# Performance work log

Measured on AMD Instinct MI355X. Metric: run time of the kernel, lower is better.

The kernel has to match this reference:

```python
import jax, jax.numpy as jnp
import numpy as np

# graph structure constants
G = 64            # num graphs
NPG = 1600        # nodes per graph
N = G * NPG       # 102400 total nodes
EPG = 51200       # edges per graph (avg degree 32)
E = G * EPG       # 3276800 total edges
F_IN = 512
H_OUT = 512
RATIO = 0.8
K = int(np.ceil(RATIO * NPG))   # 1280 kept nodes per graph
NK = G * K


def gcn_conv(x, src, dst, W, b, n, ew):
    """PyG GCNConv: D^-1/2 (A+I) D^-1/2 X W + b, with edge weights ew."""
    h = x @ W
    deg = jax.ops.segment_sum(ew, dst, num_segments=n) + 1.0  # +1 for self loop
    dis = jax.lax.rsqrt(deg)
    norm = dis[src] * dis[dst] * ew                 # [E]
    agg = jax.ops.segment_sum(h[src] * norm[:, None], dst, num_segments=n)
    return agg + h * (dis * dis)[:, None] + b       # self-loop norm = dis_i^2


def setup_inputs() -> dict:
    key = jax.random.key(0)
    k_x, k_e, k_w1, k_wr, k_wo, k_w2 = jax.random.split(key, 6)
    x = jax.random.normal(k_x, (N, F_IN), dtype=jnp.float32)
    # within-graph random edges
    local = jax.random.randint(k_e, (2, G, EPG), 0, NPG, dtype=jnp.int32)
    offs = (jnp.arange(G, dtype=jnp.int32) * NPG)[None, :, None]
    edge_index = (local + offs).reshape(2, E)
    batch = jnp.repeat(jnp.arange(G, dtype=jnp.int32), NPG)
    W1 = jax.random.normal(k_w1, (F_IN, 16), dtype=jnp.float32) * (1.0 / np.sqrt(F_IN))
    b1 = jnp.zeros((16,), jnp.float32)
    Wrel = jax.random.normal(k_wr, (16, 1), dtype=jnp.float32) * 0.25
    brel = jnp.zeros((1,), jnp.float32)
    Wroot = jax.random.normal(k_wo, (16, 1), dtype=jnp.float32) * 0.25
    W2 = jax.random.normal(k_w2, (16, H_OUT), dtype=jnp.float32) * 0.25
    b2 = jnp.zeros((H_OUT,), jnp.float32)
    return {"x": x, "edge_index": edge_index, "batch": batch,
            "W1": W1, "b1": b1, "Wrel": Wrel, "brel": brel,
            "Wroot": Wroot, "W2": W2, "b2": b2}


def reference(x, edge_index, batch, W1, b1, Wrel, brel, Wroot, W2, b2):
    src, dst = edge_index[0], edge_index[1]
    ones_e = jnp.ones((E,), x.dtype)
    # conv1 + relu
    h1 = jax.nn.relu(gcn_conv(x, src, dst, W1, b1, N, ones_e))   # [N,16]
    # SAGPooling score: GraphConv(16,1) = lin_rel(sum_j x_j) + lin_root(x), then tanh
    agg = jax.ops.segment_sum(h1[src], dst, num_segments=N)
    score = jnp.tanh((agg @ Wrel + brel + h1 @ Wroot)[:, 0])      # [N]
    # per-graph top-k (graphs are equal-sized, contiguous)
    vals, idx = jax.lax.top_k(score.reshape(G, NPG), K)           # [G,K]
    perm = (idx + (jnp.arange(G, dtype=idx.dtype) * NPG)[:, None]).reshape(-1)  # [NK]
    xk = h1[perm] * vals.reshape(-1)[:, None]                     # x[perm] * score[perm]
    # filter_adj: keep edges with both endpoints kept, remap indices
    kept = jnp.zeros((N,), bool).at[perm].set(True)
    inv = jnp.zeros((N,), jnp.int32).at[perm].set(jnp.arange(NK, dtype=jnp.int32))
    em = (kept[src] & kept[dst]).astype(x.dtype)                  # weight-0 == dropped edge
    # conv2 + relu on pooled graph
    h2 = jax.nn.relu(gcn_conv(xk, inv[src], inv[dst], W2, b2, NK, em))  # [NK,H]
    # global mean pool (each graph keeps exactly K nodes)
    out = jax.ops.segment_sum(h2, batch[perm], num_segments=G) / K
    return out
```

## Files before the change

### kernel.cpp

```cpp
#include <hip/hip_runtime.h>
#include <math.h>

#define G_    64
#define NPG_  1600
#define N_    (G_*NPG_)
#define EPG_  51200
#define E_    (G_*EPG_)
#define FIN_  512
#define HOUT_ 512
#define KEEP_ 1280

__global__ __launch_bounds__(1024) void k_build(const int* __restrict__ esrc,
                                                const int* __restrict__ edst,
                                                int* __restrict__ offs,
                                                int* __restrict__ rend,
                                                float* __restrict__ dis,
                                                unsigned short* __restrict__ csr) {
  __shared__ __align__(16) unsigned short csrs[EPG_];
  __shared__ int hist[NPG_];
  __shared__ int wsum[16];
  const int g = blockIdx.x, t = threadIdx.x;
  const int lane = t & 63, wid = t >> 6;
  const int eb = g * EPG_, nb = g * NPG_;

  for (int i = t; i < NPG_; i += 1024) hist[i] = 0;
  __syncthreads();
  for (int e = t; e < EPG_; e += 1024) atomicAdd(&hist[edst[eb + e] - nb], 1);
  __syncthreads();

  int c0 = 0, c1 = 0;
  if (t < 800) { c0 = hist[2 * t]; c1 = hist[2 * t + 1]; }
  const int val = c0 + c1;
  int incl = val;
#pragma unroll
  for (int m = 1; m < 64; m <<= 1) {
    const int u = __shfl_up(incl, m);
    if (lane >= m) incl += u;
  }
  if (lane == 63) wsum[wid] = incl;
  __syncthreads();
  int woff = 0;
  for (int w2 = 0; w2 < wid; ++w2) woff += wsum[w2];
  incl += woff;
  if (t < 800) {
    const int excl = incl - val;
    const int p0 = excl, p1 = p0 + c0;
    offs[nb + 2 * t] = eb + p0;     rend[nb + 2 * t] = eb + p1;
    offs[nb + 2 * t + 1] = eb + p1; rend[nb + 2 * t + 1] = eb + p1 + c1;
    dis[nb + 2 * t] = rsqrtf((float)c0 + 1.0f);
    dis[nb + 2 * t + 1] = rsqrtf((float)c1 + 1.0f);
    hist[2 * t] = p0;
    hist[2 * t + 1] = p1;
  }
  __syncthreads();
  for (int e = t; e < EPG_; e += 1024) {
    const int s = esrc[eb + e];
    const int d = edst[eb + e] - nb;
    const int p = atomicAdd(&hist[d], 1);
    csrs[p] = (unsigned short)(s - nb);
  }
  __syncthreads();
  const uint4* s4 = reinterpret_cast<const uint4*>(csrs);
  uint4* d4 = reinterpret_cast<uint4*>(csr + eb);
  for (int i = t; i < EPG_ / 8; i += 1024) d4[i] = s4[i];
}

typedef _Float16 f16x8 __attribute__((ext_vector_type(8)));
typedef float f32x4 __attribute__((ext_vector_type(4)));
#define WSTR_ 520

__global__ __launch_bounds__(256, 4) void k_xw1(const float* __restrict__ x,
                                                const float* __restrict__ W1,
                                                const float* __restrict__ dis,
                                                float* __restrict__ hd) {
  __shared__ _Float16 wls[2][16][WSTR_];
  const int t = threadIdx.x;

  for (int i = t; i < FIN_ * 16; i += 256) {
    const int k = i >> 4, n = i & 15;
    const float w = W1[i];
    const _Float16 w1 = (_Float16)w;
    const float r = w - (float)w1;
    wls[0][n][k] = w1;
    wls[1][n][k] = (_Float16)r;
  }
  __syncthreads();

  const int lane = t & 63, wid = t >> 6;
  const int g = lane >> 4, m = lane & 15;
  const int tile = blockIdx.x * 4 + wid;
  const int rb = tile * 16;

  const float* xrow = x + (size_t)(rb + m) * FIN_ + g * 8;
  const _Float16* wb1 = &wls[0][m][g * 8];
  const _Float16* wb2 = &wls[1][m][g * 8];

  f32x4 acc = {0.f, 0.f, 0.f, 0.f};
#pragma unroll
  for (int t4 = 0; t4 < 16; ++t4) {
    const float4 p0 = *reinterpret_cast<const float4*>(xrow + t4 * 32);
    const float4 p1 = *reinterpret_cast<const float4*>(xrow + t4 * 32 + 4);
    const float xv[8] = {p0.x, p0.y, p0.z, p0.w, p1.x, p1.y, p1.z, p1.w};
    f16x8 a1, a2;
#pragma unroll
    for (int j = 0; j < 8; ++j) {
      const _Float16 h = (_Float16)xv[j];
      a1[j] = h;
      a2[j] = (_Float16)(xv[j] - (float)h);
    }
    const f16x8 b1 = *reinterpret_cast<const f16x8*>(wb1 + t4 * 32);
    const f16x8 b2 = *reinterpret_cast<const f16x8*>(wb2 + t4 * 32);
    acc = __builtin_amdgcn_mfma_f32_16x16x32_f16(a1, b1, acc, 0, 0, 0);
    acc = __builtin_amdgcn_mfma_f32_16x16x32_f16(a1, b2, acc, 0, 0, 0);
    acc = __builtin_amdgcn_mfma_f32_16x16x32_f16(a2, b1, acc, 0, 0, 0);
  }

  const float4 d4 = reinterpret_cast<const float4*>(dis)[(rb >> 2) + g];
  const float dd[4] = {d4.x, d4.y, d4.z, d4.w};
#pragma unroll
  for (int rg = 0; rg < 4; ++rg)
    hd[(size_t)(rb + g * 4 + rg) * 16 + m] = acc[rg] * dd[rg];
}

__global__ __launch_bounds__(1024) void k_conv1l(
    const unsigned short* __restrict__ csr, const int* __restrict__ offs,
    const int* __restrict__ rend, const float* __restrict__ hd,
    const float* __restrict__ dis, const float* __restrict__ b1,
    const float* __restrict__ Wrel, const float* __restrict__ Wroot,
    float* __restrict__ h1, float* __restrict__ rarr, float* __restrict__ tarr) {
  __shared__ float hds[NPG_ * 16];
  const int g = blockIdx.x >> 2, q = blockIdx.x & 3;
  const int nb = g * NPG_;
  const int t = threadIdx.x;
  {
    const float4* src = reinterpret_cast<const float4*>(hd + (size_t)nb * 16);
    float4* dst = reinterpret_cast<float4*>(hds);
    for (int i = t; i < NPG_ * 4; i += 1024) dst[i] = src[i];
  }
  __syncthreads();
  const int c = t & 15;
  const float bb = b1[c], wr = Wrel[c], wo = Wroot[c];
  const int vend = q * 400 + 400;
  for (int vl = q * 400 + (t >> 4); vl < vend; vl += 64) {
    const int v = nb + vl;
    const int rs = offs[v], re = rend[v];
    float acc = 0.f;
    int k = rs;
    for (; k + 4 <= re; k += 4) {
      const int s0 = csr[k], s1 = csr[k + 1];
      const int s2 = csr[k + 2], s3 = csr[k + 3];
      acc += hds[s0 * 16 + c] + hds[s1 * 16 + c];
      acc += hds[s2 * 16 + c] + hds[s3 * 16 + c];
    }
    for (; k < re; ++k) acc += hds[csr[k] * 16 + c];
    const float dd = dis[v];
    float val = fmaf(acc + hds[vl * 16 + c], dd, bb);
    val = fmaxf(val, 0.f);
    h1[(size_t)v * 16 + c] = val;
    float r = val * wr;
    float tt = val * wo;
#pragma unroll
    for (int m = 1; m < 16; m <<= 1) {
      r += __shfl_xor(r, m);
      tt += __shfl_xor(tt, m);
    }
    if (c == 0) { rarr[v] = r; tarr[v] = tt; }
  }
}

__global__ __launch_bounds__(320) void k_score(
    const unsigned short* __restrict__ csr, const int* __restrict__ offs,
    const int* __restrict__ rend, const float* __restrict__ rarr,
    const float* __restrict__ tarr, const float* __restrict__ brel,
    float* __restrict__ scoreg, unsigned* __restrict__ uug) {
  __shared__ float rar[NPG_];
  const int g = blockIdx.x / 5, q = blockIdx.x % 5;
  const int nb = g * NPG_;
  const int t = threadIdx.x;
  for (int i = t; i < NPG_; i += 320) rar[i] = rarr[nb + i];
  __syncthreads();
  const int vl = q * 320 + t;
  const int v = nb + vl;
  const int rs = offs[v], re = rend[v];
  float sum = 0.f;
  int k = rs;
  for (; k + 4 <= re; k += 4) {
    sum += rar[csr[k]] + rar[csr[k + 1]];
    sum += rar[csr[k + 2]] + rar[csr[k + 3]];
  }
  for (; k < re; ++k) sum += rar[csr[k]];
  const float s = tanhf(sum + brel[0] + tarr[v]);
  scoreg[v] = s;
  const unsigned ub = __float_as_uint(s);
  uug[v] = (ub & 0x80000000u) ? ~ub : (ub | 0x80000000u);
}

__global__ __launch_bounds__(1024) void k_topk(
    const unsigned* __restrict__ uug, int* __restrict__ kept,
    float* __restrict__ out) {
  __shared__ unsigned uu[NPG_];
  __shared__ int kp[NPG_];
  __shared__ int hist[256];
  __shared__ int part[16];
  __shared__ int scal[2];
  const int g = blockIdx.x, t = threadIdx.x;
  const int lane = t & 63, wid = t >> 6;
  const int nb = g * NPG_;

  for (int i = t; i < NPG_; i += 1024) uu[i] = uug[nb + i];
  if (t == 0) { scal[0] = 0; scal[1] = KEEP_; }
  __syncthreads();

  const unsigned maskTab[4] = {0u, 0xFF000000u, 0xFFFF0000u, 0xFFFFFF00u};
  const int shTab[4] = {24, 16, 8, 0};
  for (int pass = 0; pass < 4; ++pass) {
    const unsigned lo = (unsigned)scal[0];
    const int remc = scal[1];
    const unsigned msk = maskTab[pass];
    const int sh = shTab[pass];
    if (t < 256) hist[t] = 0;
    __syncthreads();
    for (int v = t; v < NPG_; v += 1024) {
      const unsigned u = uu[v];
      if (((u ^ lo) & msk) == 0) atomicAdd(&hist[(u >> sh) & 255], 1);
    }
    __syncthreads();
    int hv = 0;
    if (t < 256) hv = hist[t];
    int incl = hv;
#pragma unroll
    for (int m = 1; m < 64; m <<= 1) {
      const int u2 = __shfl_up(incl, m);
      if (lane >= m) incl += u2;
    }
    if (t < 256 && lane == 63) part[wid] = incl;
    __syncthreads();
    if (t < 256) {
      int woff = 0;
      for (int w2 = 0; w2 < wid; ++w2) woff += part[w2];
      const int tot = part[0] + part[1] + part[2] + part[3];
      const int sb = tot - (incl + woff) + hv;
      const int sb1 = sb - hv;
      if (sb >= remc && sb1 < remc) {
        scal[0] = (int)(lo | ((unsigned)t << sh));
        scal[1] = remc - sb1;
      }
    }
    __syncthreads();
  }
  const unsigned T = (unsigned)scal[0];
  const int remT = scal[1];

  const int i0 = 2 * t, i1 = 2 * t + 1;
  int f0 = 0, f1 = 0;
  if (i0 < NPG_) f0 = (uu[i0] == T);
  if (i1 < NPG_) f1 = (uu[i1] == T);
  int incl2 = f0 + f1;
#pragma unroll
  for (int m = 1; m < 64; m <<= 1) {
    const int u2 = __shfl_up(incl2, m);
    if (lane >= m) incl2 += u2;
  }
  if (lane == 63) part[wid] = incl2;
  __syncthreads();
  int woff2 = 0;
  for (int w2 = 0; w2 < wid; ++w2) woff2 += part[w2];
  const int excl = incl2 + woff2 - (f0 + f1);
  if (i0 < NPG_) kp[i0] = (uu[i0] > T) || (f0 && excl < remT);
  if (i1 < NPG_) kp[i1] = (uu[i1] > T) || (f1 && (excl + f0) < remT);
  __syncthreads();
  for (int v = t; v < NPG_; v += 1024) kept[nb + v] = kp[v];
  if (t < HOUT_) out[g * HOUT_ + t] = 0.f;
}

__global__ __launch_bounds__(320) void k_post(
    const unsigned short* __restrict__ csr, const int* __restrict__ offs,
    const int* __restrict__ rend, const int* __restrict__ kept,
    const float* __restrict__ scoreg, const float* __restrict__ h1,
    float* __restrict__ dis2, float* __restrict__ h1w) {
  __shared__ int kp[NPG_];
  __shared__ float wvs[320];
  const int g = blockIdx.x / 5, q = blockIdx.x % 5;
  const int nb = g * NPG_;
  const int t = threadIdx.x;
  for (int i = t; i < NPG_; i += 320) kp[i] = kept[nb + i];
  __syncthreads();
  const int vl = q * 320 + t;
  const int v = nb + vl;
  float w = 0.f;
  if (kp[vl]) {
    const int rs = offs[v], re = rend[v];
    int c2 = 0, k = rs;
    for (; k + 4 <= re; k += 4) {
      c2 += kp[csr[k]] + kp[csr[k + 1]];
      c2 += kp[csr[k + 2]] + kp[csr[k + 3]];
    }
    for (; k < re; ++k) c2 += kp[csr[k]];
    const float d2 = rsqrtf((float)c2 + 1.0f);
    dis2[v] = d2;
    w = scoreg[v] * d2;
  }
  wvs[t] = w;
  __syncthreads();
  const size_t base = (size_t)(nb + q * 320) * 16;
  for (int i = t; i < 320 * 16; i += 320)
    h1w[base + i] = h1[base + i] * wvs[i >> 4];
}

__global__ __launch_bounds__(1024) void k_conv2l(
    const unsigned short* __restrict__ csr, const int* __restrict__ offs,
    const int* __restrict__ rend, const float* __restrict__ h1w,
    const int* __restrict__ kept, const float* __restrict__ dis2,
    float* __restrict__ y16) {
  __shared__ float hds[NPG_ * 16];
  const int g = blockIdx.x >> 2, q = blockIdx.x & 3;
  const int nb = g * NPG_;
  const int t = threadIdx.x;
  {
    const float4* src = reinterpret_cast<const float4*>(h1w + (size_t)nb * 16);
    float4* dst = reinterpret_cast<float4*>(hds);
    for (int i = t; i < NPG_ * 4; i += 1024) dst[i] = src[i];
  }
  __syncthreads();
  const int c = t & 15;
  const int vend = q * 400 + 400;
  for (int vl = q * 400 + (t >> 4); vl < vend; vl += 64) {
    const int v = nb + vl;
    if (!kept[v]) continue;
    const int rs = offs[v], re = rend[v];
    float acc = 0.f;
    int k = rs;
    for (; k + 4 <= re; k += 4) {
      const int s0 = csr[k], s1 = csr[k + 1];
      const int s2 = csr[k + 2], s3 = csr[k + 3];
      acc += hds[s0 * 16 + c] + hds[s1 * 16 + c];
      acc += hds[s2 * 16 + c] + hds[s3 * 16 + c];
    }
    for (; k < re; ++k) acc += hds[csr[k] * 16 + c];
    acc += hds[vl * 16 + c];
    y16[(size_t)v * 16 + c] = acc * dis2[v];
  }
}

__global__ __launch_bounds__(256, 1) void k_gemm2pool(const float* __restrict__ y16,
                                                      const int* __restrict__ kept,
                                                      const float* __restrict__ W2,
                                                      const float* __restrict__ b2,
                                                      float* __restrict__ out) {
  __shared__ float red[256];
  const int blk = blockIdx.x;
  const int g = blk >> 5;
  const int sub = blk & 31;
  const int jbase = (sub & 1) * 256;
  const int nstart = g * NPG_ + (sub >> 1) * 100;
  const int tid = threadIdx.x;
  const int wave = tid >> 6, lane = tid & 63;

  float w[16][4];
#pragma unroll
  for (int k = 0; k < 16; ++k)
#pragma unroll
    for (int c = 0; c < 4; ++c)
      w[k][c] = W2[k * HOUT_ + jbase + lane + c * 64];
  float b2r[4];
#pragma unroll
  for (int c = 0; c < 4; ++c) b2r[c] = b2[jbase + lane + c * 64];

  float acc[4] = {0.f, 0.f, 0.f, 0.f};
  for (int i = wave; i < 100; i += 4) {
    const int v = nstart + i;
    if (!kept[v]) continue;
    const float4* yp = reinterpret_cast<const float4*>(y16 + (size_t)v * 16);
    float4 q0 = yp[0], q1 = yp[1], q2 = yp[2], q3 = yp[3];
    const float yv[16] = {q0.x, q0.y, q0.z, q0.w, q1.x, q1.y, q1.z, q1.w,
                          q2.x, q2.y, q2.z, q2.w, q3.x, q3.y, q3.z, q3.w};
    float z[4] = {b2r[0], b2r[1], b2r[2], b2r[3]};
#pragma unroll
    for (int k = 0; k < 16; ++k)
#pragma unroll
      for (int c = 0; c < 4; ++c)
        z[c] = fmaf(yv[k], w[k][c], z[c]);
#pragma unroll
    for (int c = 0; c < 4; ++c) acc[c] += fmaxf(z[c], 0.f);
  }

  red[tid] = 0.f;
  __syncthreads();
#pragma unroll
  for (int c = 0; c < 4; ++c) atomicAdd(&red[lane + 64 * c], acc[c]);
  __syncthreads();
  atomicAdd(&out[g * HOUT_ + jbase + tid], red[tid] * (1.0f / (float)KEEP_));
}

extern "C" void kernel_launch(void* const* d_in, const int* in_sizes, int n_in,
                              void* d_out, int out_size, void* d_ws, size_t ws_size,
                              hipStream_t stream) {
  (void)in_sizes; (void)n_in; (void)out_size; (void)ws_size;
  const float* x     = (const float*)d_in[0];
  const int*   ei    = (const int*)  d_in[1];
  const float* W1    = (const float*)d_in[3];
  const float* b1    = (const float*)d_in[4];
  const float* Wrel  = (const float*)d_in[5];
  const float* brel  = (const float*)d_in[6];
  const float* Wroot = (const float*)d_in[7];
  const float* W2    = (const float*)d_in[8];
  const float* b2    = (const float*)d_in[9];
  const int* esrc = ei;
  const int* edst = ei + E_;

  char* ws = (char*)d_ws;
  float*          hd     = (float*)(ws);
  unsigned*       uug    = (unsigned*)(ws);
  float*          scoreg = (float*)(ws + 409600);
  float*          h1     = (float*)(ws + 6553600);
  float*          h1w    = (float*)(ws + 13107200);
  float*          y16    = (float*)(ws + 19660800);
  unsigned short* csr    = (unsigned short*)(ws + 26214400);
  int*            offs   = (int*)(ws + 32768000);
  int*            rendp  = (int*)(ws + 33177600);
  float*          dis    = (float*)(ws + 33587200);
  int*            kept   = (int*)(ws + 33996800);
  float*          rarr   = (float*)(ws + 34406400);
  float*          tarr   = (float*)(ws + 34816000);
  float*          dis2   = (float*)(ws + 35225600);
  float*          out    = (float*)d_out;

  hipLaunchKernelGGL(k_build,     dim3(G_),    dim3(1024), 0, stream,
                     esrc, edst, offs, rendp, dis, csr);
  hipLaunchKernelGGL(k_xw1,       dim3(1600),  dim3(256),  0, stream,
                     x, W1, dis, hd);
  hipLaunchKernelGGL(k_conv1l,    dim3(256),   dim3(1024), 0, stream,
                     csr, offs, rendp, hd, dis, b1, Wrel, Wroot, h1, rarr, tarr);
  hipLaunchKernelGGL(k_score,     dim3(320),   dim3(320),  0, stream,
                     csr, offs, rendp, rarr, tarr, brel, scoreg, uug);
  hipLaunchKernelGGL(k_topk,      dim3(G_),    dim3(1024), 0, stream,
                     uug, kept, out);
  hipLaunchKernelGGL(k_post,      dim3(320),   dim3(320),  0, stream,
                     csr, offs, rendp, kept, scoreg, h1, dis2, h1w);
  hipLaunchKernelGGL(k_conv2l,    dim3(256),   dim3(1024), 0, stream,
                     csr, offs, rendp, h1w, kept, dis2, y16);
  hipLaunchKernelGGL(k_gemm2pool, dim3(2048),  dim3(256),  0, stream,
                     y16, kept, W2, b2, out);
}
```

Before: 214.3 us.

## Fuse CSR build and X·W1 GEMM into one block-specialized kernel

CSR construction and the first feature GEMM now run in a single launch. The first 64 blocks build the per-graph CSR and degree normalizers, while the remaining blocks compute x·W1 with split-fp16 MFMA. Because the GEMM no longer waits for the degree result, the dis scaling moves into conv1's shared-memory staging load. This removes the serialization and one launch, letting the edge-sort work overlap the bandwidth-bound GEMM. In exchange, the shared-memory union sized for the CSR buffer applies to GEMM blocks too, which may limit how many of them fit per CU.

```diff
diff --git a/kernel.cpp b/kernel.cpp
--- a/kernel.cpp
+++ b/kernel.cpp
@@ -10,116 +10,119 @@
 #define HOUT_ 512
 #define KEEP_ 1280
 
-__global__ __launch_bounds__(1024) void k_build(const int* __restrict__ esrc,
-                                                const int* __restrict__ edst,
-                                                int* __restrict__ offs,
-                                                int* __restrict__ rend,
-                                                float* __restrict__ dis,
-                                                unsigned short* __restrict__ csr) {
-  __shared__ __align__(16) unsigned short csrs[EPG_];
-  __shared__ int hist[NPG_];
-  __shared__ int wsum[16];
-  const int g = blockIdx.x, t = threadIdx.x;
-  const int lane = t & 63, wid = t >> 6;
-  const int eb = g * EPG_, nb = g * NPG_;
-
-  for (int i = t; i < NPG_; i += 1024) hist[i] = 0;
-  __syncthreads();
-  for (int e = t; e < EPG_; e += 1024) atomicAdd(&hist[edst[eb + e] - nb], 1);
-  __syncthreads();
-
-  int c0 = 0, c1 = 0;
-  if (t < 800) { c0 = hist[2 * t]; c1 = hist[2 * t + 1]; }
-  const int val = c0 + c1;
-  int incl = val;
-#pragma unroll
-  for (int m = 1; m < 64; m <<= 1) {
-    const int u = __shfl_up(incl, m);
-    if (lane >= m) incl += u;
-  }
-  if (lane == 63) wsum[wid] = incl;
-  __syncthreads();
-  int woff = 0;
-  for (int w2 = 0; w2 < wid; ++w2) woff += wsum[w2];
-  incl += woff;
-  if (t < 800) {
-    const int excl = incl - val;
-    const int p0 = excl, p1 = p0 + c0;
-    offs[nb + 2 * t] = eb + p0;     rend[nb + 2 * t] = eb + p1;
-    offs[nb + 2 * t + 1] = eb + p1; rend[nb + 2 * t + 1] = eb + p1 + c1;
-    dis[nb + 2 * t] = rsqrtf((float)c0 + 1.0f);
-    dis[nb + 2 * t + 1] = rsqrtf((float)c1 + 1.0f);
-    hist[2 * t] = p0;
-    hist[2 * t + 1] = p1;
-  }
-  __syncthreads();
-  for (int e = t; e < EPG_; e += 1024) {
-    const int s = esrc[eb + e];
-    const int d = edst[eb + e] - nb;
-    const int p = atomicAdd(&hist[d], 1);
-    csrs[p] = (unsigned short)(s - nb);
-  }
-  __syncthreads();
-  const uint4* s4 = reinterpret_cast<const uint4*>(csrs);
-  uint4* d4 = reinterpret_cast<uint4*>(csr + eb);
-  for (int i = t; i < EPG_ / 8; i += 1024) d4[i] = s4[i];
-}
-
 typedef _Float16 f16x8 __attribute__((ext_vector_type(8)));
 typedef float f32x4 __attribute__((ext_vector_type(4)));
 #define WSTR_ 520
 
-__global__ __launch_bounds__(256, 4) void k_xw1(const float* __restrict__ x,
-                                                const float* __restrict__ W1,
-                                                const float* __restrict__ dis,
-                                                float* __restrict__ hd) {
-  __shared__ _Float16 wls[2][16][WSTR_];
+union BXShared {
+  struct {
+    unsigned short csrs[EPG_];
+    int hist[NPG_];
+    int wsum[16];
+  } b;
+  struct {
+    _Float16 wls[2][16][WSTR_];
+  } x;
+};
+
+__global__ __launch_bounds__(1024, 4) void k_bx(
+    const int* __restrict__ esrc, const int* __restrict__ edst,
+    int* __restrict__ offs, int* __restrict__ rend,
+    float* __restrict__ dis, unsigned short* __restrict__ csr,
+    const float* __restrict__ x, const float* __restrict__ W1,
+    float* __restrict__ hd) {
+  __shared__ BXShared sm;
   const int t = threadIdx.x;
-
-  for (int i = t; i < FIN_ * 16; i += 256) {
-    const int k = i >> 4, n = i & 15;
-    const float w = W1[i];
-    const _Float16 w1 = (_Float16)w;
-    const float r = w - (float)w1;
-    wls[0][n][k] = w1;
-    wls[1][n][k] = (_Float16)r;
-  }
-  __syncthreads();
-
   const int lane = t & 63, wid = t >> 6;
-  const int g = lane >> 4, m = lane & 15;
-  const int tile = blockIdx.x * 4 + wid;
-  const int rb = tile * 16;
-
-  const float* xrow = x + (size_t)(rb + m) * FIN_ + g * 8;
-  const _Float16* wb1 = &wls[0][m][g * 8];
-  const _Float16* wb2 = &wls[1][m][g * 8];
-
-  f32x4 acc = {0.f, 0.f, 0.f, 0.f};
-#pragma unroll
-  for (int t4 = 0; t4 < 16; ++t4) {
-    const float4 p0 = *reinterpret_cast<const float4*>(xrow + t4 * 32);
-    const float4 p1 = *reinterpret_cast<const float4*>(xrow + t4 * 32 + 4);
-    const float xv[8] = {p0.x, p0.y, p0.z, p0.w, p1.x, p1.y, p1.z, p1.w};
-    f16x8 a1, a2;
-#pragma unroll
-    for (int j = 0; j < 8; ++j) {
-      const _Float16 h = (_Float16)xv[j];
-      a1[j] = h;
-      a2[j] = (_Float16)(xv[j] - (float)h);
-    }
-    const f16x8 b1 = *reinterpret_cast<const f16x8*>(wb1 + t4 * 32);
-    const f16x8 b2 = *reinterpret_cast<const f16x8*>(wb2 + t4 * 32);
-    acc = __builtin_amdgcn_mfma_f32_16x16x32_f16(a1, b1, acc, 0, 0, 0);
-    acc = __builtin_amdgcn_mfma_f32_16x16x32_f16(a1, b2, acc, 0, 0, 0);
-    acc = __builtin_amdgcn_mfma_f32_16x16x32_f16(a2, b1, acc, 0, 0, 0);
-  }
-
-  const float4 d4 = reinterpret_cast<const float4*>(dis)[(rb >> 2) + g];
-  const float dd[4] = {d4.x, d4.y, d4.z, d4.w};
-#pragma unroll
-  for (int rg = 0; rg < 4; ++rg)
-    hd[(size_t)(rb + g * 4 + rg) * 16 + m] = acc[rg] * dd[rg];
+
+  if (blockIdx.x < 64) {
+    const int g = blockIdx.x;
+    const int eb = g * EPG_, nb = g * NPG_;
+
+    for (int i = t; i < NPG_; i += 1024) sm.b.hist[i] = 0;
+    __syncthreads();
+    for (int e = t; e < EPG_; e += 1024)
+      atomicAdd(&sm.b.hist[edst[eb + e] - nb], 1);
+    __syncthreads();
+
+    int c0 = 0, c1 = 0;
+    if (t < 800) { c0 = sm.b.hist[2 * t]; c1 = sm.b.hist[2 * t + 1]; }
+    const int val = c0 + c1;
+    int incl = val;
+#pragma unroll
+    for (int m = 1; m < 64; m <<= 1) {
+      const int u = __shfl_up(incl, m);
+      if (lane >= m) incl += u;
+    }
+    if (lane == 63) sm.b.wsum[wid] = incl;
+    __syncthreads();
+    int woff = 0;
+    for (int w2 = 0; w2 < wid; ++w2) woff += sm.b.wsum[w2];
+    incl += woff;
+    if (t < 800) {
+      const int excl = incl - val;
+      const int p0 = excl, p1 = p0 + c0;
+      offs[nb + 2 * t] = eb + p0;     rend[nb + 2 * t] = eb + p1;
+      offs[nb + 2 * t + 1] = eb + p1; rend[nb + 2 * t + 1] = eb + p1 + c1;
+      dis[nb + 2 * t] = rsqrtf((float)c0 + 1.0f);
+      dis[nb + 2 * t + 1] = rsqrtf((float)c1 + 1.0f);
+      sm.b.hist[2 * t] = p0;
+      sm.b.hist[2 * t + 1] = p1;
+    }
+    __syncthreads();
+    for (int e = t; e < EPG_; e += 1024) {
+      const int s = esrc[eb + e];
+      const int d = edst[eb + e] - nb;
+      const int p = atomicAdd(&sm.b.hist[d], 1);
+      sm.b.csrs[p] = (unsigned short)(s - nb);
+    }
+    __syncthreads();
+    const uint4* s4 = reinterpret_cast<const uint4*>(sm.b.csrs);
+    uint4* d4 = reinterpret_cast<uint4*>(csr + eb);
+    for (int i = t; i < EPG_ / 8; i += 1024) d4[i] = s4[i];
+  } else {
+    for (int i = t; i < FIN_ * 16; i += 1024) {
+      const int k = i >> 4, n = i & 15;
+      const float w = W1[i];
+      const _Float16 w1 = (_Float16)w;
+      const float r = w - (float)w1;
+      sm.x.wls[0][n][k] = w1;
+      sm.x.wls[1][n][k] = (_Float16)r;
+    }
+    __syncthreads();
+
+    const int g = lane >> 4, m = lane & 15;
+    const int tile = (blockIdx.x - 64) * 16 + wid;
+    const int rb = tile * 16;
+
+    const float* xrow = x + (size_t)(rb + m) * FIN_ + g * 8;
+    const _Float16* wb1 = &sm.x.wls[0][m][g * 8];
+    const _Float16* wb2 = &sm.x.wls[1][m][g * 8];
+
+    f32x4 acc = {0.f, 0.f, 0.f, 0.f};
+#pragma unroll
+    for (int t4 = 0; t4 < 16; ++t4) {
+      const float4 p0 = *reinterpret_cast<const float4*>(xrow + t4 * 32);
+      const float4 p1 = *reinterpret_cast<const float4*>(xrow + t4 * 32 + 4);
+      const float xv[8] = {p0.x, p0.y, p0.z, p0.w, p1.x, p1.y, p1.z, p1.w};
+      f16x8 a1, a2;
+#pragma unroll
+      for (int j = 0; j < 8; ++j) {
+        const _Float16 h = (_Float16)xv[j];
+        a1[j] = h;
+        a2[j] = (_Float16)(xv[j] - (float)h);
+      }
+      const f16x8 b1 = *reinterpret_cast<const f16x8*>(wb1 + t4 * 32);
+      const f16x8 b2 = *reinterpret_cast<const f16x8*>(wb2 + t4 * 32);
+      acc = __builtin_amdgcn_mfma_f32_16x16x32_f16(a1, b1, acc, 0, 0, 0);
+      acc = __builtin_amdgcn_mfma_f32_16x16x32_f16(a1, b2, acc, 0, 0, 0);
+      acc = __builtin_amdgcn_mfma_f32_16x16x32_f16(a2, b1, acc, 0, 0, 0);
+    }
+
+#pragma unroll
+    for (int rg = 0; rg < 4; ++rg)
+      hd[(size_t)(rb + g * 4 + rg) * 16 + m] = acc[rg];
+  }
 }
 
 __global__ __launch_bounds__(1024) void k_conv1l(
@@ -135,7 +138,11 @@
   {
     const float4* src = reinterpret_cast<const float4*>(hd + (size_t)nb * 16);
     float4* dst = reinterpret_cast<float4*>(hds);
-    for (int i = t; i < NPG_ * 4; i += 1024) dst[i] = src[i];
+    for (int i = t; i < NPG_ * 4; i += 1024) {
+      const float4 v = src[i];
+      const float dd = dis[nb + (i >> 2)];
+      dst[i] = make_float4(v.x * dd, v.y * dd, v.z * dd, v.w * dd);
+    }
   }
   __syncthreads();
   const int c = t & 15;
@@ -425,10 +432,8 @@
   float*          dis2   = (float*)(ws + 35225600);
   float*          out    = (float*)d_out;
 
-  hipLaunchKernelGGL(k_build,     dim3(G_),    dim3(1024), 0, stream,
-                     esrc, edst, offs, rendp, dis, csr);
-  hipLaunchKernelGGL(k_xw1,       dim3(1600),  dim3(256),  0, stream,
-                     x, W1, dis, hd);
+  hipLaunchKernelGGL(k_bx,        dim3(464),   dim3(1024), 0, stream,
+                     esrc, edst, offs, rendp, dis, csr, x, W1, hd);
   hipLaunchKernelGGL(k_conv1l,    dim3(256),   dim3(1024), 0, stream,
                      csr, offs, rendp, hd, dis, b1, Wrel, Wroot, h1, rarr, tarr);
   hipLaunchKernelGGL(k_score,     dim3(320),   dim3(320),  0, stream,
```

Measured after the change: 186.1 us, median of 2. -13.1%, faster.
